# Performance work log

Measured on AMD Instinct MI355X. Metric: run time of the kernel, lower is better.

Reference implementation:

```python
import jax, jax.numpy as jnp
import numpy as np

H, U = 64, 64  # matrix-completion patch size; system size is (H*U)^2 = 4096^2


def svtC(X, tau):
    # Singular value thresholding: soft-threshold singular values by tau.
    u, s, vt = jnp.linalg.svd(X, full_matrices=False)
    return (u * jax.nn.relu(s - tau)) @ vt


def setup_inputs() -> dict:
    key = jax.random.key(0)
    ks = jax.random.split(key, 12)
    x = jax.random.normal(ks[0], (H, U), jnp.float32)
    L = jax.random.normal(ks[1], (H, U), jnp.float32)
    entries_mask = jax.random.randint(ks[2], (H, U), 0, 2).astype(bool)
    # D_tilda: symmetric PSD (HU, HU) smoothness operator so the system is well-conditioned
    M = jax.random.normal(ks[3], (H * U, H * U), jnp.float32)
    D_tilda = (M @ M.T) / jnp.float32(H * U)
    th_P = jax.random.normal(ks[4], (H, U), jnp.float32)
    v = jax.random.normal(ks[5], (), jnp.float32)
    coef_gamma = jax.random.uniform(ks[6], (), jnp.float32)
    neta = jax.random.uniform(ks[7], (), jnp.float32)
    lamda1 = jax.random.uniform(ks[8], (), jnp.float32)
    lamda2 = jax.random.uniform(ks[9], (), jnp.float32)
    rho = jax.random.uniform(ks[10], (), jnp.float32) + jnp.float32(0.1)
    S = jax.random.normal(ks[11], (H, H), jnp.float32) / np.float32(np.sqrt(H))
    return {"x": x, "L": L, "entries_mask": entries_mask, "D_tilda": D_tilda,
            "th_P": th_P, "v": v, "coef_gamma": coef_gamma, "neta": neta,
            "lamda1": lamda1, "lamda2": lamda2, "rho": rho, "S": S}


def reference(x, L, entries_mask, D_tilda, th_P, v, coef_gamma, neta,
              lamda1, lamda2, rho, S):
    tau = jax.nn.sigmoid(v) * coef_gamma
    # Q_tilda = diag(vec(mask)); S_tilda = kron(I_U, S^T S)
    q = entries_mask.astype(jnp.float32).reshape(-1)  # (HU,)
    StS = S.T @ S                                      # (H, H)
    S_tilda = jnp.kron(jnp.eye(U, dtype=jnp.float32), StS)  # (HU, HU)
    eye = jnp.eye(H * U, dtype=jnp.float32)
    A = jnp.diag(q) + lamda1 * D_tilda + lamda2 * S_tilda + rho * eye
    vec = rho * (L - th_P) + jnp.where(entries_mask, x, jnp.float32(0.0))
    # Original uses explicit dense inverse followed by matvec
    Xtmp = (jnp.linalg.inv(A) @ vec.reshape(-1)).reshape(H, U)
    Ltmp = svtC(Xtmp + th_P, tau)
    Ptmp = th_P + neta * (Xtmp - Ltmp)
    return Ltmp, Ptmp
```

## Files before the change

kernel.cpp:

```cpp
#include <hip/hip_runtime.h>
#include <cstddef>

#define HU    4096
#define NBLK  256
#define NTHR  512
#define MAXIT 100
#define TOL2  1e-7f

#define WS_STS  0
#define WS_DINV 4096
#define WS_R0   8192
#define WS_U0   12288
#define WS_W    16384
#define WS_BAR  24576
#define WS_END  (WS_BAR + 2 * 256 * 2)

typedef _Float16 half4v __attribute__((ext_vector_type(4)));

__device__ __forceinline__ float fastrcp(float x) {
  float r; asm("v_rcp_f32 %0, %1" : "=v"(r) : "v"(x)); return r;
}
__device__ __forceinline__ float fastsqrt(float x) {
  float r; asm("v_sqrt_f32 %0, %1" : "=v"(r) : "v"(x)); return r;
}
__device__ __forceinline__ float fastrsq(float x) {
  float r; asm("v_rsq_f32 %0, %1" : "=v"(r) : "v"(x)); return r;
}

__device__ __forceinline__ float waveReduce(float v) {
#pragma unroll
  for (int off = 32; off > 0; off >>= 1) v += __shfl_xor(v, off, 64);
  return v;
}

__device__ __forceinline__ float blockSum(float v, float* red) {
  v = waveReduce(v);
  if ((threadIdx.x & 63) == 0) red[threadIdx.x >> 6] = v;
  __syncthreads();
  float s = 0.f;
#pragma unroll
  for (int i = 0; i < 8; ++i) s += red[i];
  __syncthreads();
  return s;
}

__device__ __forceinline__ float gsync_dk(unsigned long long* slots, unsigned gen,
                                          float* red) {
  __syncthreads();
  const int tid = threadIdx.x, lane = tid & 63;
  unsigned long long* arr = slots + (gen & 1) * 256;
  if (tid < 64) {
    if (lane == 0) {
      float s = 0.f;
#pragma unroll
      for (int i = 0; i < 8; ++i) s += red[i];
      __threadfence();
      __hip_atomic_store(&arr[blockIdx.x],
                         ((unsigned long long)gen << 32) | __float_as_uint(s),
                         __ATOMIC_RELEASE, __HIP_MEMORY_SCOPE_AGENT);
    }
    float dsum;
    for (;;) {
      const unsigned long long v0 = __hip_atomic_load(&arr[lane],
                                      __ATOMIC_RELAXED, __HIP_MEMORY_SCOPE_AGENT);
      const unsigned long long v1 = __hip_atomic_load(&arr[lane + 64],
                                      __ATOMIC_RELAXED, __HIP_MEMORY_SCOPE_AGENT);
      const unsigned long long v2 = __hip_atomic_load(&arr[lane + 128],
                                      __ATOMIC_RELAXED, __HIP_MEMORY_SCOPE_AGENT);
      const unsigned long long v3 = __hip_atomic_load(&arr[lane + 192],
                                      __ATOMIC_RELAXED, __HIP_MEMORY_SCOPE_AGENT);
      const bool ok = ((unsigned)(v0 >> 32) >= gen) && ((unsigned)(v1 >> 32) >= gen)
                   && ((unsigned)(v2 >> 32) >= gen) && ((unsigned)(v3 >> 32) >= gen);
      if (__all(ok)) {
        dsum = __uint_as_float((unsigned)v0) + __uint_as_float((unsigned)v1)
             + __uint_as_float((unsigned)v2) + __uint_as_float((unsigned)v3);
        break;
      }
      __builtin_amdgcn_s_sleep(1);
    }
    const float dk = waveReduce(dsum);
    __threadfence();
    if (lane == 0) red[0] = dk;
  }
  __syncthreads();
  const float dk = red[0];
  __syncthreads();
  return dk;
}

#define SWP 6
#define S_W 68

__device__ __forceinline__ float red16(float x) {
  int t;
  t = __builtin_amdgcn_update_dpp(0, __float_as_int(x), 0x128, 0xF, 0xF, false);
  x += __int_as_float(t);
  t = __builtin_amdgcn_update_dpp(0, __float_as_int(x), 0x124, 0xF, 0xF, false);
  x += __int_as_float(t);
  t = __builtin_amdgcn_update_dpp(0, __float_as_int(x), 0x122, 0xF, 0xF, false);
  x += __int_as_float(t);
  t = __builtin_amdgcn_update_dpp(0, __float_as_int(x), 0x121, 0xF, 0xF, false);
  x += __int_as_float(t);
  return x;
}

__device__ __forceinline__ int gf8mul(int a, int b) {
  int p = 0;
  if (b & 1) p ^= a;
  if (b & 2) p ^= (a << 1);
  if (b & 4) p ^= (a << 2);
  if (p & 16) p ^= 22;
  if (p & 8)  p ^= 11;
  return p;
}

__device__ __forceinline__ int sel8(const int c[8], int i) {
  int r = c[0];
  r = (i == 1) ? c[1] : r;
  r = (i == 2) ? c[2] : r;
  r = (i == 3) ? c[3] : r;
  r = (i == 4) ? c[4] : r;
  r = (i == 5) ? c[5] : r;
  r = (i == 6) ? c[6] : r;
  r = (i == 7) ? c[7] : r;
  return r;
}

__global__ void __launch_bounds__(NTHR, 1)
fused_kernel(const float* __restrict__ x_in, const float* __restrict__ L_in,
             const int* __restrict__ mask, const float* __restrict__ D,
             const float* __restrict__ thP, const float* __restrict__ S,
             const float* __restrict__ l1p, const float* __restrict__ l2p,
             const float* __restrict__ rhop, const float* __restrict__ vp,
             const float* __restrict__ cgp, const float* __restrict__ netap,
             float* __restrict__ ws, float* __restrict__ out)
{
  __shared__ __align__(16) float u_l[HU];
  __shared__ __align__(16) char pool[128 * 1024];
  __shared__ float red[8];
  __shared__ float g_s[64];
  unsigned long long* slots = (unsigned long long*)(ws + WS_BAR);
  const float* sts = ws + WS_STS;
  const float lam1 = *l1p, lam2 = *l2p, rho = *rhop;
  const int tid = threadIdx.x, b = blockIdx.x;
  const int wv = tid >> 6, lane = tid & 63;
  unsigned gen = 0;

  const int gtid = b * NTHR + tid;
  if (gtid < HU) {
    const int a = gtid >> 6, c = gtid & 63;
    float acc = 0.f, sdiag = 0.f;
    for (int h = 0; h < 64; ++h) {
      const float sa = S[h * 64 + a], sc = S[h * 64 + c];
      acc = fmaf(sa, sc, acc);
      sdiag = fmaf(sc, sc, sdiag);
    }
    ws[WS_STS + gtid] = acc;
    const float q = mask[gtid] ? 1.f : 0.f;
    const float diag = q + rho + lam1 * D[(size_t)gtid * (HU + 1)] + lam2 * sdiag;
    const float bb = rho * (L_in[gtid] - thP[gtid]) + (mask[gtid] ? x_in[gtid] : 0.f);
    const float di = 1.f / diag;
    ws[WS_DINV + gtid] = di;
    ws[WS_R0 + gtid] = bb;
    ws[WS_U0 + gtid] = bb * di;
  }

  {
    const float4* __restrict__ Dg = (const float4*)(D + (size_t)b * 16 * HU);
    half4v* __restrict__ Dh4 = (half4v*)pool;
    for (int o = tid; o < 16 * HU / 4; o += NTHR) {
      const float4 dv = Dg[o];
      half4v h;
      h[0] = (_Float16)dv.x; h[1] = (_Float16)dv.y;
      h[2] = (_Float16)dv.z; h[3] = (_Float16)dv.w;
      Dh4[o] = h;
    }
  }
  if (tid < 8) red[tid] = 0.f;
  gsync_dk(slots, ++gen, red);

  float r_reg[8], s_reg[8], dinv_reg[8];
  float acc0 = 0.f;
#pragma unroll
  for (int m = 0; m < 8; ++m) {
    const int i = tid + m * NTHR;
    const float rv = ws[WS_R0 + i], uv = ws[WS_U0 + i];
    r_reg[m] = rv; u_l[i] = uv; dinv_reg[m] = ws[WS_DINV + i];
    s_reg[m] = 0.f;
  }
  __syncthreads();
#pragma unroll
  for (int m = 0; m < 8; ++m) acc0 = fmaf(r_reg[m], u_l[tid + m * NTHR], acc0);
  const float gamma0 = blockSum(acc0, red);

  float p_arr[8], x_arr[8];
#pragma unroll
  for (int m = 0; m < 8; ++m) { p_arr[m] = 0.f; x_arr[m] = 0.f; }

  const int row0 = b * 16 + wv * 2;
  const int iq = row0 >> 6, j0 = row0 & 63;
  const float4* __restrict__ u4 = (const float4*)u_l;
  const float m0 = mask[row0] ? 1.f : 0.f;
  const float m1 = mask[row0 + 1] ? 1.f : 0.f;
  const float sts0 = sts[j0 * 64 + lane];
  const float sts1 = sts[j0 * 64 + 64 + lane];
  const float dex0 = D[(size_t)row0 * (HU + 1)];
  const float dex1 = D[(size_t)(row0 + 1) * (HU + 1)];
  const float diagf0 = m0 + rho + lam1 * (dex0 - (float)(_Float16)dex0);
  const float diagf1 = m1 + rho + lam1 * (dex1 - (float)(_Float16)dex1);
  const half4v* __restrict__ H0 = (const half4v*)((_Float16*)pool + (size_t)(wv * 2) * HU);
  const half4v* __restrict__ H1 = H0 + (HU / 4);

  float gamma = gamma0, gamma_prev = 1.f, alpha_prev = 1.f;
  for (int k = 0; k < MAXIT; ++k) {
    float* __restrict__ wbuf = ws + WS_W + (k & 1) * HU;
    {
      float acc_a = 0.f, acc_b = 0.f;
#pragma unroll
      for (int it = 0; it < 16; ++it) {
        const float4 uu = u4[it * 64 + lane];
        const half4v d0 = H0[it * 64 + lane];
        const half4v d1 = H1[it * 64 + lane];
        acc_a = fmaf((float)d0[0], uu.x, acc_a); acc_a = fmaf((float)d0[1], uu.y, acc_a);
        acc_a = fmaf((float)d0[2], uu.z, acc_a); acc_a = fmaf((float)d0[3], uu.w, acc_a);
        acc_b = fmaf((float)d1[0], uu.x, acc_b); acc_b = fmaf((float)d1[1], uu.y, acc_b);
        acc_b = fmaf((float)d1[2], uu.z, acc_b); acc_b = fmaf((float)d1[3], uu.w, acc_b);
      }
      const float us = u_l[iq * 64 + lane];
      float t0 = fmaf(lam1, acc_a, lam2 * (sts0 * us));
      float t1 = fmaf(lam1, acc_b, lam2 * (sts1 * us));
      t0 = waveReduce(t0);
      t1 = waveReduce(t1);
      const float u0v = u_l[row0], u1v = u_l[row0 + 1];
      const float w0 = t0 + diagf0 * u0v;
      const float w1 = t1 + diagf1 * u1v;
      if (lane == 0) {
        wbuf[row0] = w0;
        wbuf[row0 + 1] = w1;
        red[wv] = fmaf(w0, u0v, w1 * u1v);
      }
    }
    const float dk = gsync_dk(slots, ++gen, red);

    const float beta  = (k == 0) ? 0.f : gamma * fastrcp(gamma_prev);
    const float denom = (k == 0) ? dk  : (dk - beta * gamma * fastrcp(alpha_prev));
    const float alpha = gamma * fastrcp(denom);

    float acc = 0.f;
#pragma unroll
    for (int m = 0; m < 8; ++m) {
      const int i = tid + m * NTHR;
      const float uold = u_l[i];
      const float wvv = wbuf[i];
      const float sv = (k == 0) ? wvv : fmaf(beta, s_reg[m], wvv);
      s_reg[m] = sv;
      const float rv = fmaf(-alpha, sv, r_reg[m]);
      r_reg[m] = rv;
      const float uv = rv * dinv_reg[m];
      u_l[i] = uv;
      acc = fmaf(rv, uv, acc);
      if (b == 0) {
        const float pk = (k == 0) ? uold : fmaf(beta, p_arr[m], uold);
        p_arr[m] = pk;
        x_arr[m] = fmaf(alpha, pk, x_arr[m]);
      }
    }
    const float gnext = blockSum(acc, red);

    gamma_prev = gamma;
    alpha_prev = alpha;
    gamma = gnext;
    if (!(gnext > TOL2 * gamma0)) break;
  }

  if (b != 0) return;

  float* Wl = (float*)pool;
  float* Yr = Wl + 64 * S_W;
  float* T1 = Yr + 64 * S_W;
  float* Wr = T1 + 64 * S_W;
  __syncthreads();

  float t0acc = 0.f;
#pragma unroll
  for (int mm = 0; mm < 8; ++mm) {
    const int i = tid + mm * NTHR;
    const int rr = i >> 6, cc = i & 63;
    const float y = x_arr[mm] + thP[i];
    Wl[cc * S_W + rr] = y;
    Yr[rr * S_W + cc] = y;
    t0acc = fmaf(y, y, t0acc);
  }
  const float T0 = blockSum(t0acc, red);
  const float thr = 1.6e-10f * T0 * T0;

  const int team = lane >> 4;
  const int sub  = lane & 15;

  for (int sweep = 0; sweep < SWP; ++sweep) {
    float offacc = 0.f;
    for (int mr = 0; mr < 9; ++mr) {
      int cols[8];
#pragma unroll
      for (int j = 0; j < 8; ++j)
        cols[j] = (mr == 8) ? (8 * wv + j) : (8 * j + (gf8mul(mr, j) ^ wv));
      for (int r = 0; r < 7; ++r) {
        const int pi = (team == 0) ? 7 : ((r + team) % 7);
        const int qi = (team == 0) ? (r % 7) : ((r + 7 - team) % 7);
        const int cp = sel8(cols, pi);
        const int cq = sel8(cols, qi);
        float4* wp = (float4*)(Wl + cp * S_W) + sub;
        float4* wq = (float4*)(Wl + cq * S_W) + sub;
        const float4 a = *wp, bb = *wq;
        float dpp = fmaf(a.x, a.x, fmaf(a.y, a.y, fmaf(a.z, a.z, a.w * a.w)));
        float dqq = fmaf(bb.x, bb.x, fmaf(bb.y, bb.y, fmaf(bb.z, bb.z, bb.w * bb.w)));
        float dpq = fmaf(a.x, bb.x, fmaf(a.y, bb.y, fmaf(a.z, bb.z, a.w * bb.w)));
        dpp = red16(dpp); dqq = red16(dqq); dpq = red16(dpq);
        offacc = fmaf(dpq, dpq, offacc);
        if (dpq * dpq > 1e-14f * dpp * dqq) {
          const float th = (dqq - dpp) * 0.5f * fastrcp(dpq);
          const float sg = (th >= 0.f) ? 1.f : -1.f;
          const float t  = sg * fastrcp(fabsf(th) + fastsqrt(fmaf(th, th, 1.f)));
          const float c1 = fastrsq(fmaf(t, t, 1.f));
          const float s1 = t * c1;
          float4 na, nb;
          na.x = c1 * a.x - s1 * bb.x;  nb.x = s1 * a.x + c1 * bb.x;
          na.y = c1 * a.y - s1 * bb.y;  nb.y = s1 * a.y + c1 * bb.y;
          na.z = c1 * a.z - s1 * bb.z;  nb.z = s1 * a.z + c1 * bb.z;
          na.w = c1 * a.w - s1 * bb.w;  nb.w = s1 * a.w + c1 * bb.w;
          *wp = na; *wq = nb;
        }
      }
      __syncthreads();
    }
    const float tot = blockSum(offacc, red);
    if (sweep >= 2 && tot < thr) break;
  }

  if (tid < 64) {
    const float4* wc = (const float4*)(Wl + tid * S_W);
    float nn = 0.f;
#pragma unroll
    for (int i2 = 0; i2 < 16; ++i2) {
      const float4 u = wc[i2];
      nn = fmaf(u.x, u.x, fmaf(u.y, u.y, fmaf(u.z, u.z, fmaf(u.w, u.w, nn))));
    }
    const float sv = sqrtf(nn);
    const float tau = (*cgp) / (1.f + expf(-(*vp)));
    g_s[tid] = (sv > tau) ? (sv - tau) / (sv * nn) : 0.f;
  }
  __syncthreads();

  const int j = tid & 63;
  const int ib = tid >> 6;

#pragma unroll
  for (int mm = 0; mm < 8; ++mm) {
    const int k = ib + 8 * mm;
    const float4* wcol = (const float4*)(Wl + k * S_W);
    float acc = 0.f;
#pragma unroll
    for (int i4 = 0; i4 < 16; ++i4) {
      const float4 wvv = wcol[i4];
      acc = fmaf(wvv.x, Yr[(4 * i4 + 0) * S_W + j], acc);
      acc = fmaf(wvv.y, Yr[(4 * i4 + 1) * S_W + j], acc);
      acc = fmaf(wvv.z, Yr[(4 * i4 + 2) * S_W + j], acc);
      acc = fmaf(wvv.w, Yr[(4 * i4 + 3) * S_W + j], acc);
    }
    T1[k * S_W + j] = acc;
  }
  for (int o = tid; o < 4096; o += 512) {
    const int i2 = o >> 6, kk = o & 63;
    Wr[i2 * S_W + kk] = Wl[kk * S_W + i2] * g_s[kk];
  }
  __syncthreads();

  const float neta = *netap;
#pragma unroll
  for (int mm = 0; mm < 8; ++mm) {
    const int i2 = ib + 8 * mm;
    const float4* wrow = (const float4*)(Wr + i2 * S_W);
    float acc = 0.f;
#pragma unroll
    for (int k4 = 0; k4 < 16; ++k4) {
      const float4 wvv = wrow[k4];
      acc = fmaf(wvv.x, T1[(4 * k4 + 0) * S_W + j], acc);
      acc = fmaf(wvv.y, T1[(4 * k4 + 1) * S_W + j], acc);
      acc = fmaf(wvv.z, T1[(4 * k4 + 2) * S_W + j], acc);
      acc = fmaf(wvv.w, T1[(4 * k4 + 3) * S_W + j], acc);
    }
    const int o = i2 * 64 + j;
    out[o] = acc;
    out[4096 + o] = thP[o] + neta * (x_arr[mm] - acc);
  }
}

extern "C" void kernel_launch(void* const* d_in, const int* in_sizes, int n_in,
                              void* d_out, int out_size, void* d_ws, size_t ws_size,
                              hipStream_t stream)
{
  const float* x_in  = (const float*)d_in[0];
  const float* L_in  = (const float*)d_in[1];
  const int*   mask  = (const int*)d_in[2];
  const float* D     = (const float*)d_in[3];
  const float* thP   = (const float*)d_in[4];
  const float* vp    = (const float*)d_in[5];
  const float* cgp   = (const float*)d_in[6];
  const float* netap = (const float*)d_in[7];
  const float* l1p   = (const float*)d_in[8];
  const float* l2p   = (const float*)d_in[9];
  const float* rhop  = (const float*)d_in[10];
  const float* S     = (const float*)d_in[11];
  float* ws  = (float*)d_ws;
  float* out = (float*)d_out;

  hipMemsetAsync(ws + WS_BAR, 0, (WS_END - WS_BAR) * sizeof(float), stream);

  void* args[] = { (void*)&x_in, (void*)&L_in, (void*)&mask, (void*)&D, (void*)&thP,
                   (void*)&S, (void*)&l1p, (void*)&l2p, (void*)&rhop,
                   (void*)&vp, (void*)&cgp, (void*)&netap, (void*)&ws, (void*)&out };
  hipLaunchCooperativeKernel((void*)fused_kernel, dim3(NBLK), dim3(NTHR),
                             args, 0, stream);
}
```

Before: 346.3 us.

## Replace all-to-all grid barrier polling with master-block gather and broadcast flags

The grid-wide barrier used to have every block's first wave poll all 256 slots. Now block 0 alone gathers the partial sums, reduces them, and publishes the result to 8 replicated flag words; each other block polls one flag with a single thread. This cuts coherent polling traffic on the slot array but adds an extra hop, since block 0 must observe all slots before the others can see the result. The wbuf loads are also hoisted into registers ahead of the update loop.

```diff
diff --git a/kernel.cpp b/kernel.cpp
--- a/kernel.cpp
+++ b/kernel.cpp
@@ -13,7 +13,8 @@
 #define WS_U0   12288
 #define WS_W    16384
 #define WS_BAR  24576
-#define WS_END  (WS_BAR + 2 * 256 * 2)
+#define WS_FLG  (WS_BAR + 1024)
+#define WS_END  (WS_FLG + 128)
 
 typedef _Float16 half4v __attribute__((ext_vector_type(4)));
 
@@ -44,43 +45,67 @@
   return s;
 }
 
-__device__ __forceinline__ float gsync_dk(unsigned long long* slots, unsigned gen,
-                                          float* red) {
-  __syncthreads();
-  const int tid = threadIdx.x, lane = tid & 63;
+__device__ __forceinline__ float gsync_dk(unsigned long long* slots,
+                                          unsigned long long* flgq,
+                                          unsigned gen, float* red) {
+  __syncthreads();
+  const int tid = threadIdx.x, lane = tid & 63, b = blockIdx.x;
   unsigned long long* arr = slots + (gen & 1) * 256;
-  if (tid < 64) {
-    if (lane == 0) {
-      float s = 0.f;
-#pragma unroll
-      for (int i = 0; i < 8; ++i) s += red[i];
+  if (b == 0) {
+    if (tid < 64) {
+      if (lane == 0) {
+        float s = 0.f;
+#pragma unroll
+        for (int i = 0; i < 8; ++i) s += red[i];
+        __threadfence();
+        __hip_atomic_store(&arr[0],
+                           ((unsigned long long)gen << 32) | __float_as_uint(s),
+                           __ATOMIC_RELEASE, __HIP_MEMORY_SCOPE_AGENT);
+      }
+      float dsum;
+      for (;;) {
+        const unsigned long long v0 = __hip_atomic_load(&arr[lane],
+                                        __ATOMIC_RELAXED, __HIP_MEMORY_SCOPE_AGENT);
+        const unsigned long long v1 = __hip_atomic_load(&arr[lane + 64],
+                                        __ATOMIC_RELAXED, __HIP_MEMORY_SCOPE_AGENT);
+        const unsigned long long v2 = __hip_atomic_load(&arr[lane + 128],
+                                        __ATOMIC_RELAXED, __HIP_MEMORY_SCOPE_AGENT);
+        const unsigned long long v3 = __hip_atomic_load(&arr[lane + 192],
+                                        __ATOMIC_RELAXED, __HIP_MEMORY_SCOPE_AGENT);
+        const bool ok = ((unsigned)(v0 >> 32) >= gen) && ((unsigned)(v1 >> 32) >= gen)
+                     && ((unsigned)(v2 >> 32) >= gen) && ((unsigned)(v3 >> 32) >= gen);
+        if (__all(ok)) {
+          dsum = __uint_as_float((unsigned)v0) + __uint_as_float((unsigned)v1)
+               + __uint_as_float((unsigned)v2) + __uint_as_float((unsigned)v3);
+          break;
+        }
+        __builtin_amdgcn_s_sleep(1);
+      }
+      const float dk = waveReduce(dsum);
       __threadfence();
-      __hip_atomic_store(&arr[blockIdx.x],
-                         ((unsigned long long)gen << 32) | __float_as_uint(s),
-                         __ATOMIC_RELEASE, __HIP_MEMORY_SCOPE_AGENT);
-    }
-    float dsum;
+      if (lane < 8)
+        __hip_atomic_store(&flgq[lane * 8],
+                           ((unsigned long long)gen << 32) | __float_as_uint(dk),
+                           __ATOMIC_RELEASE, __HIP_MEMORY_SCOPE_AGENT);
+      if (lane == 0) red[0] = dk;
+    }
+  } else if (tid == 0) {
+    float s = 0.f;
+#pragma unroll
+    for (int i = 0; i < 8; ++i) s += red[i];
+    __threadfence();
+    __hip_atomic_store(&arr[b],
+                       ((unsigned long long)gen << 32) | __float_as_uint(s),
+                       __ATOMIC_RELEASE, __HIP_MEMORY_SCOPE_AGENT);
+    unsigned long long* fq = flgq + (b & 7) * 8;
+    unsigned long long f;
     for (;;) {
-      const unsigned long long v0 = __hip_atomic_load(&arr[lane],
-                                      __ATOMIC_RELAXED, __HIP_MEMORY_SCOPE_AGENT);
-      const unsigned long long v1 = __hip_atomic_load(&arr[lane + 64],
-                                      __ATOMIC_RELAXED, __HIP_MEMORY_SCOPE_AGENT);
-      const unsigned long long v2 = __hip_atomic_load(&arr[lane + 128],
-                                      __ATOMIC_RELAXED, __HIP_MEMORY_SCOPE_AGENT);
-      const unsigned long long v3 = __hip_atomic_load(&arr[lane + 192],
-                                      __ATOMIC_RELAXED, __HIP_MEMORY_SCOPE_AGENT);
-      const bool ok = ((unsigned)(v0 >> 32) >= gen) && ((unsigned)(v1 >> 32) >= gen)
-                   && ((unsigned)(v2 >> 32) >= gen) && ((unsigned)(v3 >> 32) >= gen);
-      if (__all(ok)) {
-        dsum = __uint_as_float((unsigned)v0) + __uint_as_float((unsigned)v1)
-             + __uint_as_float((unsigned)v2) + __uint_as_float((unsigned)v3);
-        break;
-      }
+      f = __hip_atomic_load(fq, __ATOMIC_RELAXED, __HIP_MEMORY_SCOPE_AGENT);
+      if ((unsigned)(f >> 32) >= gen) break;
       __builtin_amdgcn_s_sleep(1);
     }
-    const float dk = waveReduce(dsum);
     __threadfence();
-    if (lane == 0) red[0] = dk;
+    red[0] = __uint_as_float((unsigned)f);
   }
   __syncthreads();
   const float dk = red[0];
@@ -140,6 +165,7 @@
   __shared__ float red[8];
   __shared__ float g_s[64];
   unsigned long long* slots = (unsigned long long*)(ws + WS_BAR);
+  unsigned long long* flgq  = (unsigned long long*)(ws + WS_FLG);
   const float* sts = ws + WS_STS;
   const float lam1 = *l1p, lam2 = *l2p, rho = *rhop;
   const int tid = threadIdx.x, b = blockIdx.x;
@@ -177,7 +203,7 @@
     }
   }
   if (tid < 8) red[tid] = 0.f;
-  gsync_dk(slots, ++gen, red);
+  gsync_dk(slots, flgq, ++gen, red);
 
   float r_reg[8], s_reg[8], dinv_reg[8];
   float acc0 = 0.f;
@@ -240,7 +266,11 @@
         red[wv] = fmaf(w0, u0v, w1 * u1v);
       }
     }
-    const float dk = gsync_dk(slots, ++gen, red);
+    const float dk = gsync_dk(slots, flgq, ++gen, red);
+
+    float wv_r[8];
+#pragma unroll
+    for (int m = 0; m < 8; ++m) wv_r[m] = wbuf[tid + m * NTHR];
 
     const float beta  = (k == 0) ? 0.f : gamma * fastrcp(gamma_prev);
     const float denom = (k == 0) ? dk  : (dk - beta * gamma * fastrcp(alpha_prev));
@@ -251,8 +281,7 @@
     for (int m = 0; m < 8; ++m) {
       const int i = tid + m * NTHR;
       const float uold = u_l[i];
-      const float wvv = wbuf[i];
-      const float sv = (k == 0) ? wvv : fmaf(beta, s_reg[m], wvv);
+      const float sv = (k == 0) ? wv_r[m] : fmaf(beta, s_reg[m], wv_r[m]);
       s_reg[m] = sv;
       const float rv = fmaf(-alpha, sv, r_reg[m]);
       r_reg[m] = rv;
```

Result: faster. 327.7 us (-5.4%).
